# Kernel optimization log

Measured on AMD Instinct MI355X. Metric: run time of the kernel, lower is better.

The kernel has to match this reference:

```python
import jax, jax.numpy as jnp
import numpy as np


def setup_inputs() -> dict:
    key = jax.random.key(0)
    k1, k2 = jax.random.split(key)
    N, D, C = 65536, 512, 64
    embeddings = jax.random.normal(k1, (N, D), dtype=jnp.float32)
    labels = jax.random.randint(k2, (N,), 0, C, dtype=jnp.int64)
    return {"embeddings": embeddings, "labels": labels, "num_classes": C}


def reference(embeddings, labels, num_classes):
    # Per-class mean (prototypes) via segment reductions. Labels are assumed
    # to be 0..C-1 with all classes present, so unique(labels) == arange(C)
    # and local_labels == labels (faithful to the torch loop in that regime).
    ones = jnp.ones(labels.shape, dtype=embeddings.dtype)
    counts = jax.ops.segment_sum(ones, labels, num_segments=num_classes)  # [C]
    sums = jax.ops.segment_sum(embeddings, labels, num_segments=num_classes)  # [C, D]
    prototypes = sums / counts[:, None]

    # Euclidean cdist: ||e||^2 + ||p||^2 - 2 e.p^T, clamped for numerical safety
    e2 = jnp.sum(embeddings * embeddings, axis=1, keepdims=True)  # [N, 1]
    p2 = jnp.sum(prototypes * prototypes, axis=1)  # [C]
    cross = embeddings @ prototypes.T  # [N, C]
    d2 = jnp.maximum(e2 + p2[None, :] - 2.0 * cross, 1e-12)
    logits = -jnp.sqrt(d2)  # [N, C], negative distances

    log_probs = jax.nn.log_softmax(logits, axis=1)
    n = labels.shape[0]
    nll = -log_probs[jnp.arange(n), labels]
    loss = jnp.mean(nll)
    accuracy = jnp.mean((jnp.argmax(logits, axis=1) == labels).astype(jnp.float32))
    return (loss, accuracy)
```

## Files before the change

### kernel.cpp

```cpp
#include <hip/hip_runtime.h>
#include <math.h>

#define NROWS 65536
#define DIM   512
#define NCLS  64
#define CCAP  1280

typedef __attribute__((ext_vector_type(4))) float f32x4;
typedef __attribute__((ext_vector_type(8))) short s16x8;

#define WS_PROTOSUM 0
#define WS_CURSORS  32768
#define WS_LOSS     32832
#define WS_ACC      32833
#define WS_DONE     32834
#define WS_P2       32836
#define WS_PERM     32912
#define WS_PBF      114944
#define MEMSET_WORDS 32835

static __device__ __forceinline__ unsigned short f2bf(float f) {
    unsigned int u = __float_as_uint(f);
    u += 0x7FFF + ((u >> 16) & 1);
    return (unsigned short)(u >> 16);
}
static __device__ __forceinline__ float bf2f(unsigned short h) {
    return __uint_as_float(((unsigned int)h) << 16);
}

__global__ __launch_bounds__(256) void k_scatter(const int* __restrict__ labels,
                                                 int* __restrict__ cursors,
                                                 int* __restrict__ perm) {
    __shared__ int lh[NCLS], lb[NCLS];
    int t = threadIdx.x;
    if (t < NCLS) lh[t] = 0;
    __syncthreads();
    int i = blockIdx.x * 256 + t;
    int lab = labels[i];
    int rank = atomicAdd(&lh[lab], 1);
    __syncthreads();
    if (t < NCLS) lb[t] = atomicAdd(&cursors[t], lh[t]);
    __syncthreads();
    int pos = lb[lab] + rank;
    if (pos < CCAP) perm[lab * CCAP + pos] = i;
}

__global__ __launch_bounds__(256) void k_psum(const float* __restrict__ emb,
                                              const int* __restrict__ cursors,
                                              const int* __restrict__ perm,
                                              float* __restrict__ protoSum) {
    __shared__ int permS[CCAP];
    __shared__ float4 red[256];
    int t   = threadIdx.x;
    int c   = blockIdx.x >> 5;
    int sub = blockIdx.x & 31;
    int dc  = sub & 3;
    int rs  = sub >> 2;
    int tl  = t & 31;
    int g   = t >> 5;

    int cnt = cursors[c];
    int n = (cnt < CCAP) ? cnt : CCAP;
    for (int i = t; i < n; i += 256) permS[i] = perm[c * CCAP + i];
    __syncthreads();

    const float4* eb = (const float4*)emb + dc * 32 + tl;
    float4 acc = make_float4(0.f, 0.f, 0.f, 0.f);
#pragma unroll 4
    for (int i = rs * 8 + g; i < n; i += 64) {
        int r = permS[i];
        float4 v = eb[(size_t)r * 128];
        acc.x += v.x; acc.y += v.y; acc.z += v.z; acc.w += v.w;
    }
    red[t] = acc;
    __syncthreads();
    if (t < 32) {
        float4 s = red[t];
#pragma unroll
        for (int gg = 1; gg < 8; ++gg) {
            float4 v = red[gg * 32 + t];
            s.x += v.x; s.y += v.y; s.z += v.z; s.w += v.w;
        }
        float* dst = &protoSum[(size_t)c * DIM + dc * 128 + t * 4];
        atomicAdd(dst + 0, s.x);
        atomicAdd(dst + 1, s.y);
        atomicAdd(dst + 2, s.z);
        atomicAdd(dst + 3, s.w);
    }
}

__global__ __launch_bounds__(512) void k_protofin(const float* __restrict__ protoSum,
                                                  const int* __restrict__ cursors,
                                                  unsigned short* __restrict__ pBf,
                                                  float* __restrict__ p2) {
    int c = blockIdx.x, d = threadIdx.x;
    float mean = protoSum[(size_t)c * DIM + d] / (float)cursors[c];
    unsigned short mb = f2bf(mean);
    int kc = d >> 5, quad = (d >> 3) & 3, j = d & 7;
    int nt = c >> 4, l15 = c & 15;
    pBf[(size_t)(((kc * 4 + quad) * 4 + nt) * 16 + l15) * 8 + j] = mb;
    float mf = bf2f(mb);
    float sq = mf * mf;
#pragma unroll
    for (int o = 32; o > 0; o >>= 1) sq += __shfl_down(sq, o, 64);
    __shared__ float red[8];
    if ((d & 63) == 0) red[d >> 6] = sq;
    __syncthreads();
    if (d == 0) {
        float ss = 0.f;
#pragma unroll
        for (int w = 0; w < 8; ++w) ss += red[w];
        p2[c] = ss;
    }
}

#define LROWS 64
#define LGRID (NROWS / LROWS)
__global__ __launch_bounds__(256) void k_logits(const float* __restrict__ emb,
                                                const int* __restrict__ labels,
                                                const unsigned short* __restrict__ pBf,
                                                const float* __restrict__ p2,
                                                float* __restrict__ lossAcc,
                                                float* __restrict__ accAcc,
                                                unsigned int* __restrict__ doneCnt,
                                                float* __restrict__ out) {
    __shared__ __align__(16) unsigned short Asm[2][LROWS * 36];
    __shared__ float e2s[LROWS];
    __shared__ float rb[8];

    int t    = threadIdx.x;
    int lane = t & 63;
    int wv   = t >> 6;
    int quad = lane >> 4;
    int l15  = lane & 15;
    int rbase = blockIdx.x * LROWS;

    f32x4 acc[4];
#pragma unroll
    for (int nt = 0; nt < 4; ++nt) acc[nt] = (f32x4){0.f, 0.f, 0.f, 0.f};
    float e2a0 = 0.f, e2a1 = 0.f;

    const float4* emb4 = (const float4*)(emb + (size_t)rbase * DIM);
    int row0 = t >> 3, j0 = t & 7;
    int row1 = 32 + row0;

    float4 g0 = emb4[(size_t)row0 * 128 + j0];
    float4 g1 = emb4[(size_t)row1 * 128 + j0];
    s16x8 bf[4];
#pragma unroll
    for (int nt = 0; nt < 4; ++nt)
        bf[nt] = *(const s16x8*)(pBf + (size_t)((quad * 4 + nt) * 16 + l15) * 8);

#pragma unroll 4
    for (int kc = 0; kc < 16; ++kc) {
        int buf = kc & 1;
        e2a0 += g0.x * g0.x + g0.y * g0.y + g0.z * g0.z + g0.w * g0.w;
        e2a1 += g1.x * g1.x + g1.y * g1.y + g1.z * g1.z + g1.w * g1.w;
        ushort4 h0, h1;
        h0.x = f2bf(g0.x); h0.y = f2bf(g0.y); h0.z = f2bf(g0.z); h0.w = f2bf(g0.w);
        h1.x = f2bf(g1.x); h1.y = f2bf(g1.y); h1.z = f2bf(g1.z); h1.w = f2bf(g1.w);
        *(ushort4*)&Asm[buf][row0 * 36 + j0 * 4] = h0;
        *(ushort4*)&Asm[buf][row1 * 36 + j0 * 4] = h1;

        float4 n0, n1; s16x8 nb[4];
        if (kc < 15) {
            n0 = emb4[(size_t)row0 * 128 + (kc + 1) * 8 + j0];
            n1 = emb4[(size_t)row1 * 128 + (kc + 1) * 8 + j0];
#pragma unroll
            for (int nt = 0; nt < 4; ++nt)
                nb[nt] = *(const s16x8*)(pBf +
                    (size_t)((((kc + 1) * 4 + quad) * 4 + nt) * 16 + l15) * 8);
        }

        asm volatile("s_waitcnt lgkmcnt(0)\n\ts_barrier" ::: "memory");

        s16x8 a = *(const s16x8*)&Asm[buf][(wv * 16 + l15) * 36 + quad * 8];
#pragma unroll
        for (int nt = 0; nt < 4; ++nt)
            acc[nt] = __builtin_amdgcn_mfma_f32_16x16x32_bf16(a, bf[nt], acc[nt], 0, 0, 0);

        g0 = n0; g1 = n1;
#pragma unroll
        for (int nt = 0; nt < 4; ++nt) bf[nt] = nb[nt];
    }

    float v0 = e2a0;
    v0 += __shfl_xor(v0, 1, 64); v0 += __shfl_xor(v0, 2, 64); v0 += __shfl_xor(v0, 4, 64);
    float v1 = e2a1;
    v1 += __shfl_xor(v1, 1, 64); v1 += __shfl_xor(v1, 2, 64); v1 += __shfl_xor(v1, 4, 64);
    if ((lane & 7) == 0) {
        e2s[wv * 8 + (lane >> 3)]      = v0;
        e2s[32 + wv * 8 + (lane >> 3)] = v1;
    }
    __syncthreads();

    float nlls = 0.f, corr = 0.f;
#pragma unroll
    for (int reg = 0; reg < 4; ++reg) {
        int rloc = wv * 16 + quad * 4 + reg;
        float e2v = e2s[rloc];
        float lg[4];
#pragma unroll
        for (int nt = 0; nt < 4; ++nt) {
            float d2 = e2v + p2[nt * 16 + l15] - 2.f * acc[nt][reg];
            d2 = fmaxf(d2, 1e-12f);
            lg[nt] = -sqrtf(d2);
        }
        float mv = lg[0]; int mc = l15;
#pragma unroll
        for (int nt = 1; nt < 4; ++nt) {
            int cix = nt * 16 + l15;
            if (lg[nt] > mv) { mv = lg[nt]; mc = cix; }
        }
#pragma unroll
        for (int o = 1; o < 16; o <<= 1) {
            float mo = __shfl_xor(mv, o, 64);
            int   co = __shfl_xor(mc, o, 64);
            if (mo > mv || (mo == mv && co < mc)) { mv = mo; mc = co; }
        }
        int lab = labels[rbase + rloc];
        float se = 0.f, ll = 0.f;
#pragma unroll
        for (int nt = 0; nt < 4; ++nt) se += __expf(lg[nt] - mv);
        if ((lab & 15) == l15) ll = lg[lab >> 4];
#pragma unroll
        for (int o = 1; o < 16; o <<= 1) {
            se += __shfl_xor(se, o, 64);
            ll += __shfl_xor(ll, o, 64);
        }
        if (l15 == 0) {
            nlls += __logf(se) + mv - ll;
            corr += (mc == lab) ? 1.f : 0.f;
        }
    }
#pragma unroll
    for (int o = 1; o < 64; o <<= 1) {
        nlls += __shfl_xor(nlls, o, 64);
        corr += __shfl_xor(corr, o, 64);
    }
    if (lane == 0) { rb[wv] = nlls; rb[4 + wv] = corr; }
    __syncthreads();
    if (t == 0) {
        atomicAdd(lossAcc, rb[0] + rb[1] + rb[2] + rb[3]);
        atomicAdd(accAcc, rb[4] + rb[5] + rb[6] + rb[7]);
        __threadfence();
        unsigned int tk = atomicAdd(doneCnt, 1u);
        if (tk == LGRID - 1) {
            float ls  = atomicAdd(lossAcc, 0.f);
            float as_ = atomicAdd(accAcc, 0.f);
            out[0] = ls * (1.f / NROWS);
            out[1] = as_ * (1.f / NROWS);
        }
    }
}

extern "C" void kernel_launch(void* const* d_in, const int* in_sizes, int n_in,
                              void* d_out, int out_size, void* d_ws, size_t ws_size,
                              hipStream_t stream) {
    const float* emb    = (const float*)d_in[0];
    const int*   labels = (const int*)d_in[1];
    float* out = (float*)d_out;

    float* wsf = (float*)d_ws;
    int*   wsi = (int*)d_ws;
    float*          protoSum = wsf + WS_PROTOSUM;
    int*            cursors  = wsi + WS_CURSORS;
    float*          lossAcc  = wsf + WS_LOSS;
    float*          accAcc   = wsf + WS_ACC;
    unsigned int*   doneCnt  = (unsigned int*)(wsi + WS_DONE);
    float*          p2       = wsf + WS_P2;
    int*            perm     = wsi + WS_PERM;
    unsigned short* pBf      = (unsigned short*)(wsf + WS_PBF);

    hipMemsetAsync(d_ws, 0, MEMSET_WORDS * sizeof(int), stream);

    k_scatter<<<NROWS / 256, 256, 0, stream>>>(labels, cursors, perm);
    k_psum<<<NCLS * 32, 256, 0, stream>>>(emb, cursors, perm, protoSum);
    k_protofin<<<NCLS, 512, 0, stream>>>(protoSum, cursors, pBf, p2);
    k_logits<<<LGRID, 256, 0, stream>>>(emb, labels, pBf, p2,
                                        lossAcc, accAcc, doneCnt, out);
}
```

Baseline: 270.8 us.

## Split K across wave pairs in logits kernel with smaller row tiles

The logits kernel now processes 32 rows per block instead of 64, doubling the grid. Waves are paired so each pair splits the 512-wide reduction in halves, and partial MFMA accumulators are combined through shared memory before the softmax/argmax epilogue, which runs only on half the waves. The prototype-sum loop unroll goes from 4 to 8. This raises parallelism and memory-level concurrency at the cost of an extra shared-memory reduction, more blocks, more per-block atomics, and an idle half of the waves during the epilogue.

```diff
diff --git a/kernel.cpp b/kernel.cpp
--- a/kernel.cpp
+++ b/kernel.cpp
@@ -66,7 +66,7 @@
 
     const float4* eb = (const float4*)emb + dc * 32 + tl;
     float4 acc = make_float4(0.f, 0.f, 0.f, 0.f);
-#pragma unroll 4
+#pragma unroll 8
     for (int i = rs * 8 + g; i < n; i += 64) {
         int r = permS[i];
         float4 v = eb[(size_t)r * 128];
@@ -114,7 +114,7 @@
     }
 }
 
-#define LROWS 64
+#define LROWS 32
 #define LGRID (NROWS / LROWS)
 __global__ __launch_bounds__(256) void k_logits(const float* __restrict__ emb,
                                                 const int* __restrict__ labels,
@@ -124,13 +124,16 @@
                                                 float* __restrict__ accAcc,
                                                 unsigned int* __restrict__ doneCnt,
                                                 float* __restrict__ out) {
-    __shared__ __align__(16) unsigned short Asm[2][LROWS * 36];
+    __shared__ __align__(16) unsigned short Asm[2][2][LROWS * 36];
+    __shared__ float accX[2][16][64];
     __shared__ float e2s[LROWS];
     __shared__ float rb[8];
 
     int t    = threadIdx.x;
     int lane = t & 63;
     int wv   = t >> 6;
+    int rt   = wv >> 1;
+    int kh   = wv & 1;
     int quad = lane >> 4;
     int l15  = lane & 15;
     int rbase = blockIdx.x * LROWS;
@@ -138,105 +141,120 @@
     f32x4 acc[4];
 #pragma unroll
     for (int nt = 0; nt < 4; ++nt) acc[nt] = (f32x4){0.f, 0.f, 0.f, 0.f};
-    float e2a0 = 0.f, e2a1 = 0.f;
+    float e2a = 0.f;
 
     const float4* emb4 = (const float4*)(emb + (size_t)rbase * DIM);
-    int row0 = t >> 3, j0 = t & 7;
-    int row1 = 32 + row0;
-
-    float4 g0 = emb4[(size_t)row0 * 128 + j0];
-    float4 g1 = emb4[(size_t)row1 * 128 + j0];
-    s16x8 bf[4];
+    int srow = t >> 3, sj = t & 7;
+    const float4* rp = emb4 + (size_t)srow * 128 + sj;
+
+    float4 g0 = rp[0];
+    float4 g1 = rp[64];
+    s16x8 bfc[4], bfn[4];
 #pragma unroll
     for (int nt = 0; nt < 4; ++nt)
-        bf[nt] = *(const s16x8*)(pBf + (size_t)((quad * 4 + nt) * 16 + l15) * 8);
+        bfc[nt] = *(const s16x8*)(pBf +
+            (size_t)(((kh * 8 * 4 + quad) * 4 + nt) * 16 + l15) * 8);
 
 #pragma unroll 4
-    for (int kc = 0; kc < 16; ++kc) {
-        int buf = kc & 1;
-        e2a0 += g0.x * g0.x + g0.y * g0.y + g0.z * g0.z + g0.w * g0.w;
-        e2a1 += g1.x * g1.x + g1.y * g1.y + g1.z * g1.z + g1.w * g1.w;
+    for (int c = 0; c < 8; ++c) {
+        int buf = c & 1;
+        e2a += g0.x * g0.x + g0.y * g0.y + g0.z * g0.z + g0.w * g0.w;
+        e2a += g1.x * g1.x + g1.y * g1.y + g1.z * g1.z + g1.w * g1.w;
         ushort4 h0, h1;
         h0.x = f2bf(g0.x); h0.y = f2bf(g0.y); h0.z = f2bf(g0.z); h0.w = f2bf(g0.w);
         h1.x = f2bf(g1.x); h1.y = f2bf(g1.y); h1.z = f2bf(g1.z); h1.w = f2bf(g1.w);
-        *(ushort4*)&Asm[buf][row0 * 36 + j0 * 4] = h0;
-        *(ushort4*)&Asm[buf][row1 * 36 + j0 * 4] = h1;
-
-        float4 n0, n1; s16x8 nb[4];
-        if (kc < 15) {
-            n0 = emb4[(size_t)row0 * 128 + (kc + 1) * 8 + j0];
-            n1 = emb4[(size_t)row1 * 128 + (kc + 1) * 8 + j0];
+        *(ushort4*)&Asm[buf][0][srow * 36 + sj * 4] = h0;
+        *(ushort4*)&Asm[buf][1][srow * 36 + sj * 4] = h1;
+
+        float4 n0, n1;
+        if (c < 7) {
+            n0 = rp[(c + 1) * 8];
+            n1 = rp[64 + (c + 1) * 8];
 #pragma unroll
             for (int nt = 0; nt < 4; ++nt)
-                nb[nt] = *(const s16x8*)(pBf +
-                    (size_t)((((kc + 1) * 4 + quad) * 4 + nt) * 16 + l15) * 8);
+                bfn[nt] = *(const s16x8*)(pBf +
+                    (size_t)((((kh * 8 + c + 1) * 4 + quad) * 4 + nt) * 16 + l15) * 8);
         }
 
         asm volatile("s_waitcnt lgkmcnt(0)\n\ts_barrier" ::: "memory");
 
-        s16x8 a = *(const s16x8*)&Asm[buf][(wv * 16 + l15) * 36 + quad * 8];
+        s16x8 a = *(const s16x8*)&Asm[buf][kh][(rt * 16 + l15) * 36 + quad * 8];
 #pragma unroll
         for (int nt = 0; nt < 4; ++nt)
-            acc[nt] = __builtin_amdgcn_mfma_f32_16x16x32_bf16(a, bf[nt], acc[nt], 0, 0, 0);
+            acc[nt] = __builtin_amdgcn_mfma_f32_16x16x32_bf16(a, bfc[nt], acc[nt], 0, 0, 0);
 
         g0 = n0; g1 = n1;
 #pragma unroll
-        for (int nt = 0; nt < 4; ++nt) bf[nt] = nb[nt];
-    }
-
-    float v0 = e2a0;
-    v0 += __shfl_xor(v0, 1, 64); v0 += __shfl_xor(v0, 2, 64); v0 += __shfl_xor(v0, 4, 64);
-    float v1 = e2a1;
-    v1 += __shfl_xor(v1, 1, 64); v1 += __shfl_xor(v1, 2, 64); v1 += __shfl_xor(v1, 4, 64);
-    if ((lane & 7) == 0) {
-        e2s[wv * 8 + (lane >> 3)]      = v0;
-        e2s[32 + wv * 8 + (lane >> 3)] = v1;
+        for (int nt = 0; nt < 4; ++nt) bfc[nt] = bfn[nt];
+    }
+
+    e2a += __shfl_xor(e2a, 1, 64);
+    e2a += __shfl_xor(e2a, 2, 64);
+    e2a += __shfl_xor(e2a, 4, 64);
+    if ((lane & 7) == 0) e2s[t >> 3] = e2a;
+
+    if (kh == 1) {
+#pragma unroll
+        for (int nt = 0; nt < 4; ++nt)
+#pragma unroll
+            for (int r = 0; r < 4; ++r) accX[rt][nt * 4 + r][lane] = acc[nt][r];
     }
     __syncthreads();
 
     float nlls = 0.f, corr = 0.f;
-#pragma unroll
-    for (int reg = 0; reg < 4; ++reg) {
-        int rloc = wv * 16 + quad * 4 + reg;
-        float e2v = e2s[rloc];
-        float lg[4];
-#pragma unroll
-        for (int nt = 0; nt < 4; ++nt) {
-            float d2 = e2v + p2[nt * 16 + l15] - 2.f * acc[nt][reg];
-            d2 = fmaxf(d2, 1e-12f);
-            lg[nt] = -sqrtf(d2);
-        }
-        float mv = lg[0]; int mc = l15;
-#pragma unroll
-        for (int nt = 1; nt < 4; ++nt) {
-            int cix = nt * 16 + l15;
-            if (lg[nt] > mv) { mv = lg[nt]; mc = cix; }
-        }
-#pragma unroll
-        for (int o = 1; o < 16; o <<= 1) {
-            float mo = __shfl_xor(mv, o, 64);
-            int   co = __shfl_xor(mc, o, 64);
-            if (mo > mv || (mo == mv && co < mc)) { mv = mo; mc = co; }
-        }
-        int lab = labels[rbase + rloc];
-        float se = 0.f, ll = 0.f;
-#pragma unroll
-        for (int nt = 0; nt < 4; ++nt) se += __expf(lg[nt] - mv);
-        if ((lab & 15) == l15) ll = lg[lab >> 4];
-#pragma unroll
-        for (int o = 1; o < 16; o <<= 1) {
-            se += __shfl_xor(se, o, 64);
-            ll += __shfl_xor(ll, o, 64);
-        }
-        if (l15 == 0) {
-            nlls += __logf(se) + mv - ll;
-            corr += (mc == lab) ? 1.f : 0.f;
-        }
-    }
-#pragma unroll
-    for (int o = 1; o < 64; o <<= 1) {
-        nlls += __shfl_xor(nlls, o, 64);
-        corr += __shfl_xor(corr, o, 64);
+    if (kh == 0) {
+#pragma unroll
+        for (int nt = 0; nt < 4; ++nt)
+#pragma unroll
+            for (int r = 0; r < 4; ++r) acc[nt][r] += accX[rt][nt * 4 + r][lane];
+
+        float p2r[4];
+#pragma unroll
+        for (int nt = 0; nt < 4; ++nt) p2r[nt] = p2[nt * 16 + l15];
+
+#pragma unroll
+        for (int reg = 0; reg < 4; ++reg) {
+            int rloc = rt * 16 + quad * 4 + reg;
+            float e2v = e2s[rloc];
+            float lg[4];
+#pragma unroll
+            for (int nt = 0; nt < 4; ++nt) {
+                float d2 = e2v + p2r[nt] - 2.f * acc[nt][reg];
+                d2 = fmaxf(d2, 1e-12f);
+                lg[nt] = -sqrtf(d2);
+            }
+            float mv = lg[0]; int mc = l15;
+#pragma unroll
+            for (int nt = 1; nt < 4; ++nt) {
+                int cix = nt * 16 + l15;
+                if (lg[nt] > mv) { mv = lg[nt]; mc = cix; }
+            }
+#pragma unroll
+            for (int o = 1; o < 16; o <<= 1) {
+                float mo = __shfl_xor(mv, o, 64);
+                int   co = __shfl_xor(mc, o, 64);
+                if (mo > mv || (mo == mv && co < mc)) { mv = mo; mc = co; }
+            }
+            int lab = labels[rbase + rloc];
+            float se = 0.f, ll = 0.f;
+#pragma unroll
+            for (int nt = 0; nt < 4; ++nt) se += __expf(lg[nt] - mv);
+            if ((lab & 15) == l15) ll = lg[lab >> 4];
+#pragma unroll
+            for (int o = 1; o < 16; o <<= 1) {
+                se += __shfl_xor(se, o, 64);
+                ll += __shfl_xor(ll, o, 64);
+            }
+            if (l15 == 0) {
+                nlls += __logf(se) + mv - ll;
+                corr += (mc == lab) ? 1.f : 0.f;
+            }
+        }
+#pragma unroll
+        for (int o = 1; o < 64; o <<= 1) {
+            nlls += __shfl_xor(nlls, o, 64);
+            corr += __shfl_xor(corr, o, 64);
+        }
     }
     if (lane == 0) { rb[wv] = nlls; rb[4 + wv] = corr; }
     __syncthreads();
```

Measured after the change: 312.5 us. 1.15x slower.
